# Performance work log

Measured on AMD Instinct MI355X. Metric: run time of the kernel, lower is better.

## Reference

```python
import jax, jax.numpy as jnp
import numpy as np

DIM = 256
H_GLOBAL = 8
H_LOCAL = 4  # max(1, num_heads // 2)
WINDOW = 5
HALF = WINDOW // 2
B, S = 4, 2048
EPS = 1e-5


def layer_norm(x, g, b):
    mu = jnp.mean(x, axis=-1, keepdims=True)
    var = jnp.mean(jnp.square(x - mu), axis=-1, keepdims=True)
    return (x - mu) * jax.lax.rsqrt(var + EPS) * g + b


def qkv_proj(x, in_w, in_b):
    qkv = x @ in_w.T + in_b
    return jnp.split(qkv, 3, axis=-1)


def global_mha(x, in_w, in_b, out_w, out_b, nh):
    Bq, Sq, D = x.shape
    hd = D // nh
    q, k, v = qkv_proj(x, in_w, in_b)
    q = q.reshape(Bq, Sq, nh, hd)
    k = k.reshape(Bq, Sq, nh, hd)
    v = v.reshape(Bq, Sq, nh, hd)
    scores = jnp.einsum('bqhd,bkhd->bhqk', q, k) / np.sqrt(hd).astype(np.float32)
    attn = jax.nn.softmax(scores, axis=-1)
    o = jnp.einsum('bhqk,bkhd->bqhd', attn, v).reshape(Bq, Sq, D)
    return o @ out_w.T + out_b


def local_mha(x, in_w, in_b, out_w, out_b, nh):
    # banded sliding-window attention, window = 2*HALF+1, per-query softmax
    Bq, Sq, D = x.shape
    hd = D // nh
    q, k, v = qkv_proj(x, in_w, in_b)
    kp = jnp.pad(k, ((0, 0), (HALF, HALF), (0, 0)))
    vp = jnp.pad(v, ((0, 0), (HALF, HALF), (0, 0)))
    # [B, S, W, D] windows of keys/values around each query position
    k_win = jnp.stack([kp[:, j:j + Sq] for j in range(WINDOW)], axis=2)
    v_win = jnp.stack([vp[:, j:j + Sq] for j in range(WINDOW)], axis=2)
    q = q.reshape(Bq, Sq, nh, hd)
    k_win = k_win.reshape(Bq, Sq, WINDOW, nh, hd)
    v_win = v_win.reshape(Bq, Sq, WINDOW, nh, hd)
    scores = jnp.einsum('bshd,bswhd->bshw', q, k_win) / np.sqrt(hd).astype(np.float32)
    idx = jnp.arange(Sq)[:, None] + jnp.arange(-HALF, HALF + 1)[None, :]  # [S, W]
    valid = (idx >= 0) & (idx < Sq)
    scores = jnp.where(valid[None, :, None, :], scores, -jnp.inf)
    attn = jax.nn.softmax(scores, axis=-1)
    o = jnp.einsum('bshw,bswhd->bshd', attn, v_win).reshape(Bq, Sq, D)
    return o @ out_w.T + out_b


def setup_inputs() -> dict:
    key = jax.random.key(0)
    ks = jax.random.split(key, 8)
    sc = 0.02
    d = DIM
    return {
        'x': jax.random.normal(ks[0], (B, S, d), jnp.float32),
        'g_in_w': jax.random.normal(ks[1], (3 * d, d), jnp.float32) * sc,
        'g_in_b': jnp.zeros((3 * d,), jnp.float32),
        'g_out_w': jax.random.normal(ks[2], (d, d), jnp.float32) * sc,
        'g_out_b': jnp.zeros((d,), jnp.float32),
        't_in_w': jax.random.normal(ks[3], (3 * d, d), jnp.float32) * sc,
        't_in_b': jnp.zeros((3 * d,), jnp.float32),
        't_out_w': jax.random.normal(ks[4], (d, d), jnp.float32) * sc,
        't_out_b': jnp.zeros((d,), jnp.float32),
        'fus_w1': jax.random.normal(ks[5], (2 * d, 2 * d), jnp.float32) * sc,
        'fus_b1': jnp.zeros((2 * d,), jnp.float32),
        'fus_w2': jax.random.normal(ks[6], (d, 2 * d), jnp.float32) * sc,
        'fus_b2': jnp.zeros((d,), jnp.float32),
        'ffn_w1': jax.random.normal(ks[7], (2 * d, d), jnp.float32) * sc,
        'ffn_b1': jnp.zeros((2 * d,), jnp.float32),
        'ffn_w2': jax.random.normal(jax.random.fold_in(key, 9), (d, 2 * d), jnp.float32) * sc,
        'ffn_b2': jnp.zeros((d,), jnp.float32),
        'gn_g': jnp.ones((d,), jnp.float32),
        'gn_b': jnp.zeros((d,), jnp.float32),
        'fn_g': jnp.ones((d,), jnp.float32),
        'fn_b': jnp.zeros((d,), jnp.float32),
    }


def reference(x, g_in_w, g_in_b, g_out_w, g_out_b,
              t_in_w, t_in_b, t_out_w, t_out_b,
              fus_w1, fus_b1, fus_w2, fus_b2,
              ffn_w1, ffn_b1, ffn_w2, ffn_b2,
              gn_g, gn_b, fn_g, fn_b):
    x_global = global_mha(x, g_in_w, g_in_b, g_out_w, g_out_b, H_GLOBAL)
    x_local = local_mha(x, t_in_w, t_in_b, t_out_w, t_out_b, H_LOCAL)
    x_comb = jnp.concatenate([x_global, x_local], axis=-1)
    x_fused = jax.nn.silu(x_comb @ fus_w1.T + fus_b1) @ fus_w2.T + fus_b2
    x = layer_norm(x + x_fused, gn_g, gn_b)
    x_ffn = jax.nn.silu(x @ ffn_w1.T + ffn_b1) @ ffn_w2.T + ffn_b2
    x = layer_norm(x + x_ffn, fn_g, fn_b)
    return x
```

## Files before the change

kernel.cpp:

```cpp
#include <hip/hip_runtime.h>

constexpr int Bb = 4;
constexpr int Ss = 2048;
constexpr int QSTR = 1536;

typedef __bf16 bf16x8 __attribute__((ext_vector_type(8)));
typedef __bf16 bf16x4 __attribute__((ext_vector_type(4)));
typedef float  f32x4  __attribute__((ext_vector_type(4)));
typedef unsigned int uint2v __attribute__((ext_vector_type(2)));
typedef unsigned int uint4v __attribute__((ext_vector_type(4)));

__device__ __forceinline__ void glds16(const void* g, void* l) {
    __builtin_amdgcn_global_load_lds(
        (const __attribute__((address_space(1))) unsigned int*)g,
        (__attribute__((address_space(3))) unsigned int*)l, 16, 0, 0);
}

__device__ __forceinline__ void xpose4(unsigned int& a, unsigned int& b) {
    uint2v r = __builtin_amdgcn_permlane32_swap(a, b, false, false);
    uint2v u = __builtin_amdgcn_permlane16_swap(r[0], r[1], false, false);
    a = u[0]; b = u[1];
}

__device__ __forceinline__ unsigned int exp2_pk(float a, float b) {
    float ea = __builtin_amdgcn_exp2f(a);
    float eb = __builtin_amdgcn_exp2f(b);
    unsigned int r;
    asm("v_cvt_pk_bf16_f32 %0, %1, %2" : "=v"(r) : "v"(ea), "v"(eb));
    return r;
}

__device__ __forceinline__ float silu_fast(float v) {
    return v / (1.f + __builtin_amdgcn_exp2f(-v * 1.4426950408889634f));
}

struct CvtArgs {
    const float* src[9];
    __bf16* dst[9];
    int start[10];
};

__global__ __launch_bounds__(256) void convert_all(CvtArgs a)
{
    int e = 0;
    const int bid = blockIdx.x;
#pragma unroll
    for (int i = 0; i < 8; i++) if (bid >= a.start[i + 1]) e = i + 1;
    const int idx = (bid - a.start[e]) * 256 + threadIdx.x;
    const float* s = a.src[e];
    float4 v0 = *(const float4*)&s[(size_t)idx * 8];
    float4 v1 = *(const float4*)&s[(size_t)idx * 8 + 4];
    bf16x8 o;
    o[0] = (__bf16)v0.x; o[1] = (__bf16)v0.y; o[2] = (__bf16)v0.z; o[3] = (__bf16)v0.w;
    o[4] = (__bf16)v1.x; o[5] = (__bf16)v1.y; o[6] = (__bf16)v1.z; o[7] = (__bf16)v1.w;
    *(bf16x8*)&a.dst[e][(size_t)idx * 8] = o;
}

__global__ __launch_bounds__(256) void gemm128(
    const __bf16* __restrict__ A, const __bf16* __restrict__ W,
    const float* __restrict__ bias, const float* __restrict__ bias2, int bsplit,
    __bf16* __restrict__ C, int K, int ldc)
{
    __shared__ __bf16 As[128 * 64];
    __shared__ __bf16 Ws[128 * 64];
    const int tid = threadIdx.x;
    const int lane = tid & 63;
    const int wv = tid >> 6;
    const int wm = (wv >> 1) * 64;
    const int wn = (wv & 1) * 64;
    const int qrow = lane & 15;
    const int quad = lane >> 4;
    const int n0 = blockIdx.x * 128;
    const int m0 = blockIdx.y * 128;

    f32x4 acc[4][4];
#pragma unroll
    for (int i = 0; i < 4; i++)
#pragma unroll
        for (int j = 0; j < 4; j++) acc[i][j] = {0.f, 0.f, 0.f, 0.f};

    for (int k0 = 0; k0 < K; k0 += 64) {
        __syncthreads();
#pragma unroll
        for (int i = 0; i < 4; i++) {
            const int c = (wv * 4 + i) * 64 + lane;
            const int row = c >> 3, g = c & 7;
            const int gs = (g ^ (row & 7)) * 8;
            glds16(&A[(size_t)(m0 + row) * K + k0 + gs], &As[(wv * 4 + i) * 512]);
            glds16(&W[(size_t)(n0 + row) * K + k0 + gs], &Ws[(wv * 4 + i) * 512]);
        }
        __syncthreads();
#pragma unroll
        for (int ksub = 0; ksub < 2; ksub++) {
            const int gl = ksub * 4 + quad;
            bf16x8 af[4], bf[4];
#pragma unroll
            for (int mi = 0; mi < 4; mi++) {
                const int row = wm + mi * 16 + qrow;
                af[mi] = *(const bf16x8*)&As[row * 64 + (gl ^ (row & 7)) * 8];
            }
#pragma unroll
            for (int ni = 0; ni < 4; ni++) {
                const int row = wn + ni * 16 + qrow;
                bf[ni] = *(const bf16x8*)&Ws[row * 64 + (gl ^ (row & 7)) * 8];
            }
#pragma unroll
            for (int mi = 0; mi < 4; mi++)
#pragma unroll
                for (int ni = 0; ni < 4; ni++)
                    acc[mi][ni] = __builtin_amdgcn_mfma_f32_16x16x32_bf16(
                        af[mi], bf[ni], acc[mi][ni], 0, 0, 0);
        }
    }

    float bz[4];
#pragma unroll
    for (int ni = 0; ni < 4; ni++) {
        const int n = n0 + wn + ni * 16 + qrow;
        bz[ni] = (n < bsplit) ? bias[n] : bias2[n - bsplit];
    }
#pragma unroll
    for (int mi = 0; mi < 4; mi++)
#pragma unroll
        for (int r = 0; r < 4; r++) {
            const int row = m0 + wm + mi * 16 + quad * 4 + r;
#pragma unroll
            for (int ni = 0; ni < 4; ni++) {
                float v = acc[mi][ni][r] + bz[ni];
                C[(size_t)row * ldc + n0 + wn + ni * 16 + qrow] = (__bf16)v;
            }
        }
}

template<bool SILU, bool OUT_BF16>
__global__ __launch_bounds__(256) void gemm_mid(
    const __bf16* __restrict__ A0, const __bf16* __restrict__ W0,
    const float* __restrict__ bias0, const __bf16* __restrict__ W1,
    const float* __restrict__ bias1, int nsplit, int aoff1, int coff1,
    void* __restrict__ C, int lda, int K, int ldc)
{
    __shared__ __bf16 As[64 * 128];
    __shared__ __bf16 Ws[64 * 128];
    const int tid = threadIdx.x;
    const int lane = tid & 63;
    const int wv = tid >> 6;
    const int wm = (wv >> 1) * 32;
    const int wn = (wv & 1) * 32;
    const int qrow = lane & 15;
    const int quad = lane >> 4;
    const bool second = (int)blockIdx.x >= nsplit;
    const int bx = second ? (blockIdx.x - nsplit) : blockIdx.x;
    const __bf16* A = second ? (A0 + aoff1) : A0;
    const __bf16* W = second ? W1 : W0;
    const float* bias = second ? bias1 : bias0;
    const int coff = second ? coff1 : 0;
    const int n0 = bx * 64;
    const int m0 = blockIdx.y * 64;

    f32x4 acc[2][2];
#pragma unroll
    for (int i = 0; i < 2; i++)
#pragma unroll
        for (int j = 0; j < 2; j++) acc[i][j] = {0.f, 0.f, 0.f, 0.f};

    for (int k0 = 0; k0 < K; k0 += 128) {
        __syncthreads();
#pragma unroll
        for (int i = 0; i < 4; i++) {
            const int c = (wv * 4 + i) * 64 + lane;
            const int row = c >> 4, s = c & 15;
            const int gs = ((s & 8) | ((s ^ row) & 7)) * 8;
            glds16(&A[(size_t)(m0 + row) * lda + k0 + gs], &As[(wv * 4 + i) * 512]);
            glds16(&W[(size_t)(n0 + row) * K + k0 + gs], &Ws[(wv * 4 + i) * 512]);
        }
        __syncthreads();
#pragma unroll
        for (int ksub = 0; ksub < 4; ksub++) {
            const int gl = ksub * 4 + quad;
            bf16x8 af[2], bf[2];
#pragma unroll
            for (int mi = 0; mi < 2; mi++) {
                const int row = wm + mi * 16 + qrow;
                const int s = (gl & 8) | ((gl ^ row) & 7);
                af[mi] = *(const bf16x8*)&As[row * 128 + s * 8];
            }
#pragma unroll
            for (int ni = 0; ni < 2; ni++) {
                const int row = wn + ni * 16 + qrow;
                const int s = (gl & 8) | ((gl ^ row) & 7);
                bf[ni] = *(const bf16x8*)&Ws[row * 128 + s * 8];
            }
#pragma unroll
            for (int mi = 0; mi < 2; mi++)
#pragma unroll
                for (int ni = 0; ni < 2; ni++)
                    acc[mi][ni] = __builtin_amdgcn_mfma_f32_16x16x32_bf16(
                        af[mi], bf[ni], acc[mi][ni], 0, 0, 0);
        }
    }

    float bz[2];
#pragma unroll
    for (int ni = 0; ni < 2; ni++) bz[ni] = bias[n0 + wn + ni * 16 + qrow];

#pragma unroll
    for (int mi = 0; mi < 2; mi++)
#pragma unroll
        for (int r = 0; r < 4; r++) {
            const int row = m0 + wm + mi * 16 + quad * 4 + r;
#pragma unroll
            for (int ni = 0; ni < 2; ni++) {
                float v = acc[mi][ni][r] + bz[ni];
                if (SILU) v = silu_fast(v);
                const int col = coff + n0 + wn + ni * 16 + qrow;
                if (OUT_BF16)
                    ((__bf16*)C)[(size_t)row * ldc + col] = (__bf16)v;
                else
                    ((float*)C)[(size_t)row * ldc + col] = v;
            }
        }
}

template<bool OBF>
__global__ __launch_bounds__(256) void gemm_ln(
    const __bf16* __restrict__ A, const __bf16* __restrict__ W,
    const float* __restrict__ bias, const float* __restrict__ res,
    const float* __restrict__ g, const float* __restrict__ be,
    float* __restrict__ out, __bf16* __restrict__ outb)
{
    __shared__ __bf16 As[16 * 128];
    __shared__ __bf16 Ws[256 * 128];
    __shared__ float lnp[2][16][4];
    const int tid = threadIdx.x;
    const int lane = tid & 63;
    const int wv = tid >> 6;
    const int qrow = lane & 15;
    const int quad = lane >> 4;
    const int m0 = blockIdx.x * 16;

    f32x4 acc[4];
#pragma unroll
    for (int ni = 0; ni < 4; ni++) acc[ni] = {0.f, 0.f, 0.f, 0.f};

    for (int k0 = 0; k0 < 512; k0 += 128) {
        __syncthreads();
        {
            const int c = wv * 64 + lane;
            const int row = c >> 4, s = c & 15;
            const int gs = ((s & 8) | ((s ^ row) & 7)) * 8;
            glds16(&A[(size_t)(m0 + row) * 512 + k0 + gs], &As[wv * 512]);
        }
#pragma unroll
        for (int i = 0; i < 16; i++) {
            const int c = (wv * 16 + i) * 64 + lane;
            const int row = c >> 4, s = c & 15;
            const int gs = ((s & 8) | ((s ^ row) & 7)) * 8;
            glds16(&W[(size_t)row * 512 + k0 + gs], &Ws[(wv * 16 + i) * 512]);
        }
        __syncthreads();
#pragma unroll
        for (int ksub = 0; ksub < 4; ksub++) {
            const int gl = ksub * 4 + quad;
            bf16x8 af, bf[4];
            {
                const int row = qrow;
                const int s = (gl & 8) | ((gl ^ row) & 7);
                af = *(const bf16x8*)&As[row * 128 + s * 8];
            }
#pragma unroll
            for (int ni = 0; ni < 4; ni++) {
                const int row = wv * 64 + ni * 16 + qrow;
                const int s = (gl & 8) | ((gl ^ row) & 7);
                bf[ni] = *(const bf16x8*)&Ws[row * 128 + s * 8];
            }
#pragma unroll
            for (int ni = 0; ni < 4; ni++)
                acc[ni] = __builtin_amdgcn_mfma_f32_16x16x32_bf16(
                    af, bf[ni], acc[ni], 0, 0, 0);
        }
    }

    f32x4 d[4];
#pragma unroll
    for (int ni = 0; ni < 4; ni++) {
        const int f = wv * 64 + ni * 16 + qrow;
        const float bz = bias[f];
#pragma unroll
        for (int r = 0; r < 4; r++)
            d[ni][r] = acc[ni][r] + bz + res[(size_t)(m0 + quad * 4 + r) * 256 + f];
    }

    f32x4 ps;
#pragma unroll
    for (int r = 0; r < 4; r++) ps[r] = d[0][r] + d[1][r] + d[2][r] + d[3][r];
#pragma unroll
    for (int off = 1; off <= 8; off <<= 1)
#pragma unroll
        for (int r = 0; r < 4; r++) ps[r] += __shfl_xor(ps[r], off, 64);
    if (qrow == 0)
#pragma unroll
        for (int r = 0; r < 4; r++) lnp[0][quad * 4 + r][wv] = ps[r];
    __syncthreads();
    float mu[4];
#pragma unroll
    for (int r = 0; r < 4; r++) {
        const int t = quad * 4 + r;
        mu[r] = (lnp[0][t][0] + lnp[0][t][1] + lnp[0][t][2] + lnp[0][t][3]) * (1.f / 256.f);
    }

#pragma unroll
    for (int r = 0; r < 4; r++) {
        float a0 = d[0][r] - mu[r], a1 = d[1][r] - mu[r];
        float a2 = d[2][r] - mu[r], a3 = d[3][r] - mu[r];
        ps[r] = a0 * a0 + a1 * a1 + a2 * a2 + a3 * a3;
    }
#pragma unroll
    for (int off = 1; off <= 8; off <<= 1)
#pragma unroll
        for (int r = 0; r < 4; r++) ps[r] += __shfl_xor(ps[r], off, 64);
    if (qrow == 0)
#pragma unroll
        for (int r = 0; r < 4; r++) lnp[1][quad * 4 + r][wv] = ps[r];
    __syncthreads();
    float rsv[4];
#pragma unroll
    for (int r = 0; r < 4; r++) {
        const int t = quad * 4 + r;
        float v = (lnp[1][t][0] + lnp[1][t][1] + lnp[1][t][2] + lnp[1][t][3]) * (1.f / 256.f);
        rsv[r] = rsqrtf(v + 1e-5f);
    }

#pragma unroll
    for (int ni = 0; ni < 4; ni++) {
        const int f = wv * 64 + ni * 16 + qrow;
        const float gg = g[f];
        const float bb = be[f];
#pragma unroll
        for (int r = 0; r < 4; r++) {
            const size_t idx = (size_t)(m0 + quad * 4 + r) * 256 + f;
            float o = (d[ni][r] - mu[r]) * rsv[r] * gg + bb;
            out[idx] = o;
            if (OBF) outb[idx] = (__bf16)o;
        }
    }
}

__global__ __launch_bounds__(512) void attn_fused(
    const __bf16* __restrict__ qkv, __bf16* __restrict__ Op,
    float* __restrict__ Lp, __bf16* __restrict__ acat)
{
    __shared__ __bf16 Kl[2][64 * 32];
    __shared__ __bf16 Vt[2][32 * 72];

    const int t = threadIdx.x;
    const int lane = t & 63;
    const int wv = t >> 6;

    if (blockIdx.x < 1024) {
        const int bid = blockIdx.x;
        const int sp = bid & 3;
        const int qc = (bid >> 2) & 7;
        const int h  = (bid >> 5) & 7;
        const int b  = bid >> 8;
        const int bS = b * Ss;
        const int q0 = qc * 256;

        const int qrow = lane & 15;
        const int quad = lane >> 4;
        const float cQ = 1.4426950408889634f * 0.17677669529663687f;

        bf16x8 qf[2];
#pragma unroll
        for (int tl = 0; tl < 2; tl++) {
            bf16x8 qraw = *(const bf16x8*)(qkv +
                (size_t)(bS + q0 + wv * 32 + tl * 16 + qrow) * QSTR + h * 32 + quad * 8);
#pragma unroll
            for (int i = 0; i < 8; i++) qf[tl][i] = (__bf16)((float)qraw[i] * cQ);
        }
        bf16x8 ones;
#pragma unroll
        for (int i = 0; i < 8; i++) ones[i] = (__bf16)1.0f;

        f32x4 o0[2], o1[2], lac[2];
#pragma unroll
        for (int tl = 0; tl < 2; tl++) {
            o0[tl] = {0.f, 0.f, 0.f, 0.f};
            o1[tl] = {0.f, 0.f, 0.f, 0.f};
            lac[tl] = {0.f, 0.f, 0.f, 0.f};
        }
        const f32x4 z = {0.f, 0.f, 0.f, 0.f};

        const int kc_c = wv * 64 + lane;
        const int kkey = kc_c >> 2, kdg = kc_c & 3;
        const int vkey = t & 63, vq = t >> 6;
        const int kc0 = sp * 8;

        bf16x4 vreg = *(const bf16x4*)(qkv +
            (size_t)(bS + kc0 * 64 + vkey) * QSTR + 512 + h * 32 + vq * 4);
        if (wv < 4)
            glds16(qkv + (size_t)(bS + kc0 * 64 + kkey) * QSTR + 256 + h * 32 + kdg * 8,
                   &Kl[0][wv * 512]);

        for (int i = 0; i < 8; i++) {
            const int cur = i & 1;
#pragma unroll
            for (int e = 0; e < 4; e++) Vt[cur][(vq * 4 + e) * 72 + vkey] = vreg[e];
            __syncthreads();
            const int nx = (i < 7) ? (kc0 + i + 1) : (kc0 + 7);
            vreg = *(const bf16x4*)(qkv +
                (size_t)(bS + nx * 64 + vkey) * QSTR + 512 + h * 32 + vq * 4);
            if (i < 7 && wv < 4)
                glds16(qkv + (size_t)(bS + nx * 64 + kkey) * QSTR + 256 + h * 32 + kdg * 8,
                       &Kl[1 - cur][wv * 512]);

            bf16x8 kf[4];
#pragma unroll
            for (int kg = 0; kg < 4; kg++)
                kf[kg] = *(const bf16x8*)&Kl[cur][(kg * 16 + qrow) * 32 + quad * 8];
            bf16x8 vf00 = *(const bf16x8*)&Vt[cur][qrow * 72 + quad * 8];
            bf16x8 vf01 = *(const bf16x8*)&Vt[cur][qrow * 72 + 32 + quad * 8];
            bf16x8 vf10 = *(const bf16x8*)&Vt[cur][(16 + qrow) * 72 + quad * 8];
            bf16x8 vf11 = *(const bf16x8*)&Vt[cur][(16 + qrow) * 72 + 32 + quad * 8];

#pragma unroll
            for (int tl = 0; tl < 2; tl++) {
                f32x4 s[4];
#pragma unroll
                for (int kg = 0; kg < 4; kg++)
                    s[kg] = __builtin_amdgcn_mfma_f32_16x16x32_bf16(
                        kf[kg], qf[tl], z, 0, 0, 0);
                unsigned int R[4][2];
#pragma unroll
                for (int kg = 0; kg < 4; kg++) {
                    R[kg][0] = exp2_pk(s[kg][0], s[kg][1]);
                    R[kg][1] = exp2_pk(s[kg][2], s[kg][3]);
                }
                xpose4(R[0][0], R[1][0]);
                xpose4(R[0][1], R[1][1]);
                xpose4(R[2][0], R[3][0]);
                xpose4(R[2][1], R[3][1]);
                uint4v p0u = {R[0][0], R[0][1], R[1][0], R[1][1]};
                uint4v p1u = {R[2][0], R[2][1], R[3][0], R[3][1]};
                bf16x8 pf0 = __builtin_bit_cast(bf16x8, p0u);
                bf16x8 pf1 = __builtin_bit_cast(bf16x8, p1u);

                o0[tl] = __builtin_amdgcn_mfma_f32_16x16x32_bf16(vf00, pf0, o0[tl], 0, 0, 0);
                o1[tl] = __builtin_amdgcn_mfma_f32_16x16x32_bf16(vf10, pf0, o1[tl], 0, 0, 0);
                lac[tl] = __builtin_amdgcn_mfma_f32_16x16x32_bf16(ones, pf0, lac[tl], 0, 0, 0);
                o0[tl] = __builtin_amdgcn_mfma_f32_16x16x32_bf16(vf01, pf1, o0[tl], 0, 0, 0);
                o1[tl] = __builtin_amdgcn_mfma_f32_16x16x32_bf16(vf11, pf1, o1[tl], 0, 0, 0);
                lac[tl] = __builtin_amdgcn_mfma_f32_16x16x32_bf16(ones, pf1, lac[tl], 0, 0, 0);
            }
        }

#pragma unroll
        for (int tl = 0; tl < 2; tl++) {
            const int gid = (b * 8 + h) * 2048 + q0 + wv * 32 + tl * 16 + qrow;
            __bf16* po = Op + (size_t)sp * 2097152 + (size_t)gid * 32;
            bf16x4 w0, w1;
#pragma unroll
            for (int r = 0; r < 4; r++) {
                w0[r] = (__bf16)o0[tl][r];
                w1[r] = (__bf16)o1[tl][r];
            }
            *(bf16x4*)&po[quad * 4]      = w0;
            *(bf16x4*)&po[16 + quad * 4] = w1;
            if (quad == 0) Lp[sp * 65536 + gid] = lac[tl][0];
        }
    } else {
        const int w = (blockIdx.x - 1024) * 8 + wv;
        const int g = lane >> 3;
        const int l8 = lane & 7;
        const int R = w * 8 + g;
        const int h = R & 3;
        const int s = (R >> 2) & 2047;
        const int b = R >> 13;

        float qv[8];
        {
            bf16x8 q8 = *(const bf16x8*)&qkv[(size_t)(b * Ss + s) * QSTR + 768 + h * 64 + l8 * 8];
#pragma unroll
            for (int e = 0; e < 8; e++) qv[e] = (float)q8[e];
        }

        float sc[5];
        bf16x8 v8[5];
#pragma unroll
        for (int j = 0; j < 5; j++) {
            int pos = s + j - 2;
            bool valid = (pos >= 0) && (pos < Ss);
            int cpos = valid ? pos : 0;
            const size_t rb = (size_t)(b * Ss + cpos) * QSTR;
            bf16x8 k8 = *(const bf16x8*)&qkv[rb + 1024 + h * 64 + l8 * 8];
            v8[j]     = *(const bf16x8*)&qkv[rb + 1280 + h * 64 + l8 * 8];
            float p = 0.f;
#pragma unroll
            for (int e = 0; e < 8; e++) p += qv[e] * (float)k8[e];
            p += __shfl_xor(p, 1, 64);
            p += __shfl_xor(p, 2, 64);
            p += __shfl_xor(p, 4, 64);
            sc[j] = valid ? p * 0.125f : -1e30f;
        }
        float m = sc[0];
#pragma unroll
        for (int j = 1; j < 5; j++) m = fmaxf(m, sc[j]);
        float l = 0.f;
        float o[8];
#pragma unroll
        for (int e = 0; e < 8; e++) o[e] = 0.f;
#pragma unroll
        for (int j = 0; j < 5; j++) {
            float pe = __builtin_amdgcn_exp2f((sc[j] - m) * 1.4426950408889634f);
            l += pe;
#pragma unroll
            for (int e = 0; e < 8; e++) o[e] += pe * (float)v8[j][e];
        }
        const float li = 1.f / l;
        bf16x8 r;
#pragma unroll
        for (int e = 0; e < 8; e++) r[e] = (__bf16)(o[e] * li);
        *(bf16x8*)&acat[(size_t)(b * Ss + s) * 512 + 256 + h * 64 + l8 * 8] = r;
    }
}

__global__ __launch_bounds__(256) void attn_combine(
    const __bf16* __restrict__ Op, const float* __restrict__ Lp,
    __bf16* __restrict__ acat)
{
    const int t = blockIdx.x * 256 + threadIdx.x;
    const int gid = t >> 3;
    const int dg = t & 7;
    const int b = gid >> 14;
    const int h = (gid >> 11) & 7;
    const int q = gid & 2047;

    const float li = 1.f / (Lp[gid] + Lp[65536 + gid] +
                            Lp[131072 + gid] + Lp[196608 + gid]);
    const __bf16* base = Op + (size_t)gid * 32 + dg * 4;
    bf16x4 a0 = *(const bf16x4*)&base[0];
    bf16x4 a1 = *(const bf16x4*)&base[2097152];
    bf16x4 a2 = *(const bf16x4*)&base[4194304];
    bf16x4 a3 = *(const bf16x4*)&base[6291456];
    bf16x4 r;
#pragma unroll
    for (int i = 0; i < 4; i++)
        r[i] = (__bf16)(((float)a0[i] + (float)a1[i] +
                         (float)a2[i] + (float)a3[i]) * li);
    *(bf16x4*)&acat[(size_t)(b * Ss + q) * 512 + h * 32 + dg * 4] = r;
}

extern "C" void kernel_launch(void* const* d_in, const int* in_sizes, int n_in,
                              void* d_out, int out_size, void* d_ws, size_t ws_size,
                              hipStream_t stream)
{
    const float* x      = (const float*)d_in[0];
    const float* g_in_w = (const float*)d_in[1];
    const float* g_in_b = (const float*)d_in[2];
    const float* g_out_w= (const float*)d_in[3];
    const float* g_out_b= (const float*)d_in[4];
    const float* t_in_w = (const float*)d_in[5];
    const float* t_in_b = (const float*)d_in[6];
    const float* t_out_w= (const float*)d_in[7];
    const float* t_out_b= (const float*)d_in[8];
    const float* fus_w1 = (const float*)d_in[9];
    const float* fus_b1 = (const float*)d_in[10];
    const float* fus_w2 = (const float*)d_in[11];
    const float* fus_b2 = (const float*)d_in[12];
    const float* ffn_w1 = (const float*)d_in[13];
    const float* ffn_b1 = (const float*)d_in[14];
    const float* ffn_w2 = (const float*)d_in[15];
    const float* ffn_b2 = (const float*)d_in[16];
    const float* gn_g   = (const float*)d_in[17];
    const float* gn_b   = (const float*)d_in[18];
    const float* fn_g   = (const float*)d_in[19];
    const float* fn_b   = (const float*)d_in[20];
    float* out = (float*)d_out;
    float* ws  = (float*)d_ws;

    __bf16* xb     = (__bf16*)(ws);
    __bf16* wb     = (__bf16*)(ws + 1048576);
    __bf16* qkvgl  = (__bf16*)(ws + 1638400);
    __bf16* acat   = (__bf16*)(ws + 7929856);
    __bf16* fcomb  = (__bf16*)(ws + 10027008);
    __bf16* h1     = (__bf16*)(ws + 12124160);
    float*  x2     = ws + 16318464;
    __bf16* x2b    = (__bf16*)(ws + 18415616);
    __bf16* h2     = h1;
    __bf16* Op = (__bf16*)(ws + 10027008);
    float*  Lp = ws + 18415616;

    __bf16* w_gin  = wb;
    __bf16* w_gout = wb + 393216;
    __bf16* w_tout = wb + 458752;
    __bf16* w_f1   = wb + 524288;
    __bf16* w_f2   = wb + 786432;
    __bf16* w_n1   = wb + 917504;
    __bf16* w_n2   = wb + 1048576;

    CvtArgs ca;
    ca.src[0] = x;      ca.dst[0] = xb;
    ca.src[1] = g_in_w; ca.dst[1] = w_gin;
    ca.src[2] = t_in_w; ca.dst[2] = w_gin + 196608;
    ca.src[3] = g_out_w;ca.dst[3] = w_gout;
    ca.src[4] = t_out_w;ca.dst[4] = w_tout;
    ca.src[5] = fus_w1; ca.dst[5] = w_f1;
    ca.src[6] = fus_w2; ca.dst[6] = w_f2;
    ca.src[7] = ffn_w1; ca.dst[7] = w_n1;
    ca.src[8] = ffn_w2; ca.dst[8] = w_n2;
    int st[10] = {0, 1024, 1120, 1216, 1248, 1280, 1408, 1472, 1536, 1600};
    for (int i = 0; i < 10; i++) ca.start[i] = st[i];

    convert_all<<<dim3(1600), 256, 0, stream>>>(ca);

    gemm128<<<dim3(12, 64), 256, 0, stream>>>(
        xb, w_gin, g_in_b, t_in_b, 768, qkvgl, 256, QSTR);
    attn_fused<<<dim3(1536), 512, 0, stream>>>(qkvgl, Op, Lp, acat);
    attn_combine<<<dim3(2048), 256, 0, stream>>>(Op, Lp, acat);
    gemm_mid<false, true><<<dim3(8, 128), 256, 0, stream>>>(
        acat, w_gout, g_out_b, w_tout, t_out_b, 4, 256, 256, fcomb, 512, 256, 512);
    gemm_mid<true,  true><<<dim3(8, 128), 256, 0, stream>>>(
        fcomb, w_f1, fus_b1, w_f1, fus_b1, 1 << 30, 0, 0, h1, 512, 512, 512);
    gemm_ln<true><<<dim3(512), 256, 0, stream>>>(
        h1, w_f2, fus_b2, x, gn_g, gn_b, x2, x2b);
    gemm_mid<true,  true><<<dim3(8, 128), 256, 0, stream>>>(
        x2b, w_n1, ffn_b1, w_n1, ffn_b1, 1 << 30, 0, 0, h2, 256, 256, 512);
    gemm_ln<false><<<dim3(512), 256, 0, stream>>>(
        h2, w_n2, ffn_b2, x2, fn_g, fn_b, out, nullptr);
}
```

Measured before the change: 205.4 us.

## Fuse FFN first GEMM with SiLU into the post-fusion LayerNorm kernel

Adds a gemm_ln_ffn kernel. It computes the fusion output projection, the residual add and the LayerNorm, keeps the normalized 16-token tile in shared memory as bf16, and then runs the FFN first GEMM with SiLU directly from that tile. This removes one kernel launch and the global write and re-read of the bf16 LayerNorm output x2b. In exchange each 16-row block re-streams the full FFN W1 matrix through shared memory, at low MFMA occupancy per block. The grid of the first gemm_mid launch is also doubled along y.

```diff
diff --git a/kernel.cpp b/kernel.cpp
--- a/kernel.cpp
+++ b/kernel.cpp
@@ -341,6 +341,175 @@
             float o = (d[ni][r] - mu[r]) * rsv[r] * gg + bb;
             out[idx] = o;
             if (OBF) outb[idx] = (__bf16)o;
+        }
+    }
+}
+
+__global__ __launch_bounds__(256) void gemm_ln_ffn(
+    const __bf16* __restrict__ A, const __bf16* __restrict__ W,
+    const float* __restrict__ bias, const float* __restrict__ res,
+    const float* __restrict__ g, const float* __restrict__ be,
+    float* __restrict__ out,
+    const __bf16* __restrict__ Wn1, const float* __restrict__ bn1,
+    __bf16* __restrict__ h2)
+{
+    __shared__ __bf16 As[16 * 128];
+    __shared__ __bf16 Ws[256 * 128];
+    __shared__ __bf16 Xl[16 * 264];
+    __shared__ float lnp[2][16][4];
+    const int tid = threadIdx.x;
+    const int lane = tid & 63;
+    const int wv = tid >> 6;
+    const int qrow = lane & 15;
+    const int quad = lane >> 4;
+    const int m0 = blockIdx.x * 16;
+
+    f32x4 acc[4];
+#pragma unroll
+    for (int ni = 0; ni < 4; ni++) acc[ni] = {0.f, 0.f, 0.f, 0.f};
+
+    for (int k0 = 0; k0 < 512; k0 += 128) {
+        __syncthreads();
+        {
+            const int c = wv * 64 + lane;
+            const int row = c >> 4, s = c & 15;
+            const int gs = ((s & 8) | ((s ^ row) & 7)) * 8;
+            glds16(&A[(size_t)(m0 + row) * 512 + k0 + gs], &As[wv * 512]);
+        }
+#pragma unroll
+        for (int i = 0; i < 16; i++) {
+            const int c = (wv * 16 + i) * 64 + lane;
+            const int row = c >> 4, s = c & 15;
+            const int gs = ((s & 8) | ((s ^ row) & 7)) * 8;
+            glds16(&W[(size_t)row * 512 + k0 + gs], &Ws[(wv * 16 + i) * 512]);
+        }
+        __syncthreads();
+#pragma unroll
+        for (int ksub = 0; ksub < 4; ksub++) {
+            const int gl = ksub * 4 + quad;
+            bf16x8 af, bf[4];
+            {
+                const int row = qrow;
+                const int s = (gl & 8) | ((gl ^ row) & 7);
+                af = *(const bf16x8*)&As[row * 128 + s * 8];
+            }
+#pragma unroll
+            for (int ni = 0; ni < 4; ni++) {
+                const int row = wv * 64 + ni * 16 + qrow;
+                const int s = (gl & 8) | ((gl ^ row) & 7);
+                bf[ni] = *(const bf16x8*)&Ws[row * 128 + s * 8];
+            }
+#pragma unroll
+            for (int ni = 0; ni < 4; ni++)
+                acc[ni] = __builtin_amdgcn_mfma_f32_16x16x32_bf16(
+                    af, bf[ni], acc[ni], 0, 0, 0);
+        }
+    }
+
+    f32x4 d[4];
+#pragma unroll
+    for (int ni = 0; ni < 4; ni++) {
+        const int f = wv * 64 + ni * 16 + qrow;
+        const float bz = bias[f];
+#pragma unroll
+        for (int r = 0; r < 4; r++)
+            d[ni][r] = acc[ni][r] + bz + res[(size_t)(m0 + quad * 4 + r) * 256 + f];
+    }
+
+    f32x4 ps;
+#pragma unroll
+    for (int r = 0; r < 4; r++) ps[r] = d[0][r] + d[1][r] + d[2][r] + d[3][r];
+#pragma unroll
+    for (int off = 1; off <= 8; off <<= 1)
+#pragma unroll
+        for (int r = 0; r < 4; r++) ps[r] += __shfl_xor(ps[r], off, 64);
+    if (qrow == 0)
+#pragma unroll
+        for (int r = 0; r < 4; r++) lnp[0][quad * 4 + r][wv] = ps[r];
+    __syncthreads();
+    float mu[4];
+#pragma unroll
+    for (int r = 0; r < 4; r++) {
+        const int t = quad * 4 + r;
+        mu[r] = (lnp[0][t][0] + lnp[0][t][1] + lnp[0][t][2] + lnp[0][t][3]) * (1.f / 256.f);
+    }
+#pragma unroll
+    for (int r = 0; r < 4; r++) {
+        float a0 = d[0][r] - mu[r], a1 = d[1][r] - mu[r];
+        float a2 = d[2][r] - mu[r], a3 = d[3][r] - mu[r];
+        ps[r] = a0 * a0 + a1 * a1 + a2 * a2 + a3 * a3;
+    }
+#pragma unroll
+    for (int off = 1; off <= 8; off <<= 1)
+#pragma unroll
+        for (int r = 0; r < 4; r++) ps[r] += __shfl_xor(ps[r], off, 64);
+    if (qrow == 0)
+#pragma unroll
+        for (int r = 0; r < 4; r++) lnp[1][quad * 4 + r][wv] = ps[r];
+    __syncthreads();
+    float rsv[4];
+#pragma unroll
+    for (int r = 0; r < 4; r++) {
+        const int t = quad * 4 + r;
+        float v = (lnp[1][t][0] + lnp[1][t][1] + lnp[1][t][2] + lnp[1][t][3]) * (1.f / 256.f);
+        rsv[r] = rsqrtf(v + 1e-5f);
+    }
+
+#pragma unroll
+    for (int ni = 0; ni < 4; ni++) {
+        const int f = wv * 64 + ni * 16 + qrow;
+        const float gg = g[f];
+        const float bb = be[f];
+#pragma unroll
+        for (int r = 0; r < 4; r++) {
+            const int tok = quad * 4 + r;
+            float o = (d[ni][r] - mu[r]) * rsv[r] * gg + bb;
+            out[(size_t)(m0 + tok) * 256 + f] = o;
+            Xl[tok * 264 + f] = (__bf16)o;
+        }
+    }
+
+    for (int fp = 0; fp < 4; fp++) {
+        f32x4 a2c[2];
+        a2c[0] = {0.f, 0.f, 0.f, 0.f};
+        a2c[1] = {0.f, 0.f, 0.f, 0.f};
+        for (int k0 = 0; k0 < 256; k0 += 128) {
+            __syncthreads();
+#pragma unroll
+            for (int i = 0; i < 8; i++) {
+                const int c = (wv * 8 + i) * 64 + lane;
+                const int row = c >> 4, s = c & 15;
+                const int gs = ((s & 8) | ((s ^ row) & 7)) * 8;
+                glds16(&Wn1[(size_t)(fp * 128 + row) * 256 + k0 + gs],
+                       &Ws[(wv * 8 + i) * 512]);
+            }
+            __syncthreads();
+#pragma unroll
+            for (int ksub = 0; ksub < 4; ksub++) {
+                const int gl = ksub * 4 + quad;
+                bf16x8 af = *(const bf16x8*)&Xl[qrow * 264 + k0 + gl * 8];
+                bf16x8 bf[2];
+#pragma unroll
+                for (int ni = 0; ni < 2; ni++) {
+                    const int row = wv * 32 + ni * 16 + qrow;
+                    const int s = (gl & 8) | ((gl ^ row) & 7);
+                    bf[ni] = *(const bf16x8*)&Ws[row * 128 + s * 8];
+                }
+#pragma unroll
+                for (int ni = 0; ni < 2; ni++)
+                    a2c[ni] = __builtin_amdgcn_mfma_f32_16x16x32_bf16(
+                        af, bf[ni], a2c[ni], 0, 0, 0);
+            }
+        }
+#pragma unroll
+        for (int ni = 0; ni < 2; ni++) {
+            const int f = fp * 128 + wv * 32 + ni * 16 + qrow;
+            const float bz = bn1[f];
+#pragma unroll
+            for (int r = 0; r < 4; r++) {
+                float v = silu_fast(a2c[ni][r] + bz);
+                h2[(size_t)(m0 + quad * 4 + r) * 512 + f] = (__bf16)v;
+            }
         }
     }
 }
@@ -584,7 +753,6 @@
     __bf16* fcomb  = (__bf16*)(ws + 10027008);
     __bf16* h1     = (__bf16*)(ws + 12124160);
     float*  x2     = ws + 16318464;
-    __bf16* x2b    = (__bf16*)(ws + 18415616);
     __bf16* h2     = h1;
     __bf16* Op = (__bf16*)(ws + 10027008);
     float*  Lp = ws + 18415616;
@@ -616,14 +784,12 @@
         xb, w_gin, g_in_b, t_in_b, 768, qkvgl, 256, QSTR);
     attn_fused<<<dim3(1536), 512, 0, stream>>>(qkvgl, Op, Lp, acat);
     attn_combine<<<dim3(2048), 256, 0, stream>>>(Op, Lp, acat);
-    gemm_mid<false, true><<<dim3(8, 128), 256, 0, stream>>>(
+    gemm_mid<false, true><<<dim3(8, 256), 256, 0, stream>>>(
         acat, w_gout, g_out_b, w_tout, t_out_b, 4, 256, 256, fcomb, 512, 256, 512);
     gemm_mid<true,  true><<<dim3(8, 128), 256, 0, stream>>>(
         fcomb, w_f1, fus_b1, w_f1, fus_b1, 1 << 30, 0, 0, h1, 512, 512, 512);
-    gemm_ln<true><<<dim3(512), 256, 0, stream>>>(
-        h1, w_f2, fus_b2, x, gn_g, gn_b, x2, x2b);
-    gemm_mid<true,  true><<<dim3(8, 128), 256, 0, stream>>>(
-        x2b, w_n1, ffn_b1, w_n1, ffn_b1, 1 << 30, 0, 0, h2, 256, 256, 512);
+    gemm_ln_ffn<<<dim3(512), 256, 0, stream>>>(
+        h1, w_f2, fus_b2, x, gn_g, gn_b, x2, w_n1, ffn_b1, h2);
     gemm_ln<false><<<dim3(512), 256, 0, stream>>>(
         h2, w_n2, ffn_b2, x2, fn_g, fn_b, out, nullptr);
 }
```

Result: slower. 213.7 us (+4.0%).
